# Kernel tuning notes

Measured on AMD Instinct MI355X. Metric: run time of the kernel, lower is better.

The kernel has to match this reference:

```python
import math
import jax, jax.numpy as jnp
import numpy as np

TOP_K = 2
N_EXP = 8
EVAL_CAPACITY_FACTOR = 2.0  # eval mode (module not training)
MIN_CAPACITY = 4


def _capacity(num_tokens):
    cap = math.floor(TOP_K * EVAL_CAPACITY_FACTOR * num_tokens / N_EXP)
    cap += cap % 2
    return max(cap, MIN_CAPACITY)


def setup_inputs() -> dict:
    key = jax.random.key(0)
    k1, k2 = jax.random.split(key)
    x = jax.random.normal(k1, (2, 2048, 1024), dtype=jnp.float32)
    w_g = jax.random.normal(k2, (8, 1024), dtype=jnp.float32) * 0.02
    return {"x": x, "w_g": w_g}


def reference(x, w_g):
    B, T, C = x.shape
    num_tokens = B * T
    cap = _capacity(num_tokens)  # static, derived from shapes

    # gating logits [B,T,E]
    logits = jnp.einsum('btc,ec->bte', x, w_g)

    # top-k + masked softmax (non-top-k logits -> -inf)
    top_logits, top_idx = jax.lax.top_k(logits, TOP_K)  # [B,T,K]
    masked = jnp.full_like(logits, -jnp.inf)
    masked = jnp.put_along_axis(masked, top_idx, top_logits, axis=-1, inplace=False)
    router_probs = jax.nn.softmax(masked, axis=-1)  # [B,T,E]

    # one-hot expert mask, ordered (k-major then token) for capacity ranking
    exp_mask = jax.nn.one_hot(top_idx, N_EXP, dtype=jnp.int32)       # [B,T,K,E]
    exp_mask = exp_mask.reshape(num_tokens, TOP_K, N_EXP)
    exp_mask = jnp.transpose(exp_mask, (1, 0, 2))                     # [K,tokens,E]

    # position of each assignment within its expert's queue
    exp_rank = jnp.cumsum(exp_mask.reshape(TOP_K * num_tokens, N_EXP), axis=0) - 1
    exp_rank = exp_rank.reshape(TOP_K, num_tokens, N_EXP)

    # drop assignments beyond capacity
    exp_mask = exp_mask * (exp_rank < cap).astype(jnp.int32)
    used_capacity = jnp.sum(exp_mask, axis=(0, 1))                    # [E]

    # per-assignment slot index [K,tokens]
    exp_rank = jnp.sum(exp_mask * exp_rank, axis=-1)

    rp = router_probs.reshape(num_tokens, N_EXP)[None, :, :]          # [1,tokens,E]
    exp_weights = exp_mask.astype(rp.dtype) * rp                      # [K,tokens,E]

    # one-hot over capacity slots -> combine weights [tokens,E,cap]
    exp_rank_sc = jax.nn.one_hot(exp_rank, cap, dtype=rp.dtype)       # [K,tokens,cap]
    cb_weight = jnp.sum(exp_weights[:, :, :, None] * exp_rank_sc[:, :, None, :], axis=0)
    sec_mask = cb_weight.astype(bool)
    return (used_capacity, cb_weight, sec_mask)
```

## Files before the change

kernel.cpp:

```cpp
#include <hip/hip_runtime.h>
#include <math.h>

#define TOKENS   4096
#define CDIM     1024
#define NEXP     8
#define CAP      2048
#define OUT_OFS  8
#define PER_OUT  (TOKENS * NEXP * CAP)
#define N4TOTAL  ((2 * PER_OUT + OUT_OFS) / 4)

#define GATE_BLOCKS   256
#define TOK_PER_WAVE  4
#define FILL_BLOCKS   ((N4TOTAL + 511) / 512)

__global__ __launch_bounds__(256) void fill_gate_kernel(const float* __restrict__ x,
                                                        const float* __restrict__ wg,
                                                        int*   __restrict__ top1,
                                                        int*   __restrict__ top2,
                                                        float* __restrict__ p1,
                                                        float* __restrict__ p2,
                                                        float4* __restrict__ out4) {
    if (blockIdx.x >= GATE_BLOCKS) {
        const int i = (blockIdx.x - GATE_BLOCKS) * 512 + threadIdx.x;
        const float4 z = make_float4(0.f, 0.f, 0.f, 0.f);
        if (i < N4TOTAL) out4[i] = z;
        const int i2 = i + 256;
        if (i2 < N4TOTAL) out4[i2] = z;
        return;
    }

    const int wave = threadIdx.x >> 6;
    const int lane = threadIdx.x & 63;

    for (int tt = 0; tt < TOK_PER_WAVE; ++tt) {
        const int tok = (blockIdx.x * 4 + wave) * TOK_PER_WAVE + tt;
        const float* xr = x + (size_t)tok * CDIM;

        float acc[NEXP];
#pragma unroll
        for (int e = 0; e < NEXP; ++e) acc[e] = 0.f;

#pragma unroll
        for (int i = 0; i < CDIM / 64; ++i) {
            const float xv = xr[lane + 64 * i];
#pragma unroll
            for (int e = 0; e < NEXP; ++e)
                acc[e] = fmaf(xv, wg[e * CDIM + lane + 64 * i], acc[e]);
        }
#pragma unroll
        for (int e = 0; e < NEXP; ++e) {
            float v = acc[e];
#pragma unroll
            for (int s = 32; s >= 1; s >>= 1) v += __shfl_xor(v, s, 64);
            acc[e] = v;
        }

        if (lane == 0) {
            int e1 = 0; float l1 = acc[0];
#pragma unroll
            for (int e = 1; e < NEXP; ++e)
                if (acc[e] > l1) { l1 = acc[e]; e1 = e; }
            int e2 = -1; float l2 = -INFINITY;
#pragma unroll
            for (int e = 0; e < NEXP; ++e)
                if (e != e1 && acc[e] > l2) { l2 = acc[e]; e2 = e; }
            const float ex = expf(l2 - l1);
            const float denom = 1.f + ex;
            top1[tok] = e1;
            top2[tok] = e2;
            p1[tok] = 1.f / denom;
            p2[tok] = ex / denom;
        }
    }
}

__global__ __launch_bounds__(256) void scan_scatter_kernel(const int* __restrict__ top1,
                                                           const int* __restrict__ top2,
                                                           const float* __restrict__ p1,
                                                           const float* __restrict__ p2,
                                                           float* __restrict__ out) {
    __shared__ int sr[2 * TOKENS];
    const int tid = threadIdx.x;

    if (tid < 64) {
        const int lane = tid;
        const int* __restrict__ src = (lane < 32) ? (top1 + lane * 128)
                                                  : (top2 + (lane - 32) * 128);
        int4 a[32];
#pragma unroll
        for (int i = 0; i < 32; ++i) a[i] = ((const int4*)src)[i];

        unsigned long long cnt = 0ull;
#pragma unroll
        for (int i = 0; i < 32; ++i) {
            cnt += 1ull << (a[i].x << 3);
            cnt += 1ull << (a[i].y << 3);
            cnt += 1ull << (a[i].z << 3);
            cnt += 1ull << (a[i].w << 3);
        }
        int c[NEXP];
#pragma unroll
        for (int e = 0; e < NEXP; ++e) c[e] = (int)((cnt >> (e * 8)) & 0xff);

        int off[NEXP], tot[NEXP];
#pragma unroll
        for (int e = 0; e < NEXP; ++e) {
            int v = c[e];
#pragma unroll
            for (int s = 1; s <= 32; s <<= 1) {
                const int u = __shfl_up(v, s, 64);
                if (lane >= s) v += u;
            }
            off[e] = v - c[e];
            tot[e] = __shfl(v, 63, 64);
        }

        int4* __restrict__ dst = (int4*)sr + lane * 32;
#pragma unroll
        for (int i = 0; i < 32; ++i) {
            int4 r;
            int e, rr;
            e = a[i].x; rr = 0;
#pragma unroll
            for (int ee = 0; ee < NEXP; ++ee) if (e == ee) { rr = off[ee]; off[ee] = rr + 1; }
            r.x = rr;
            e = a[i].y; rr = 0;
#pragma unroll
            for (int ee = 0; ee < NEXP; ++ee) if (e == ee) { rr = off[ee]; off[ee] = rr + 1; }
            r.y = rr;
            e = a[i].z; rr = 0;
#pragma unroll
            for (int ee = 0; ee < NEXP; ++ee) if (e == ee) { rr = off[ee]; off[ee] = rr + 1; }
            r.z = rr;
            e = a[i].w; rr = 0;
#pragma unroll
            for (int ee = 0; ee < NEXP; ++ee) if (e == ee) { rr = off[ee]; off[ee] = rr + 1; }
            r.w = rr;
            dst[i] = r;
        }

        if (lane < NEXP)
            out[lane] = (float)(tot[lane] < CAP ? tot[lane] : CAP);
    }
    __syncthreads();

    for (int a = tid; a < 2 * TOKENS; a += 256) {
        const int k = (a >= TOKENS);
        const int t = a & (TOKENS - 1);
        const int e = k ? top2[t] : top1[t];
        const int r = sr[a];
        const float p = k ? p2[t] : p1[t];
        if (r < CAP) {
            const size_t idx = ((size_t)t * NEXP + e) * CAP + r;
            out[OUT_OFS + idx] = p;
            out[OUT_OFS + (size_t)PER_OUT + idx] = (p != 0.f) ? 1.f : 0.f;
        }
    }
}

extern "C" void kernel_launch(void* const* d_in, const int* in_sizes, int n_in,
                              void* d_out, int out_size, void* d_ws, size_t ws_size,
                              hipStream_t stream) {
    const float* x  = (const float*)d_in[0];
    const float* wg = (const float*)d_in[1];
    float* out = (float*)d_out;

    int*   top1 = (int*)d_ws;
    int*   top2 = top1 + TOKENS;
    float* p1   = (float*)(top2 + TOKENS);
    float* p2   = p1 + TOKENS;

    fill_gate_kernel<<<GATE_BLOCKS + FILL_BLOCKS, 256, 0, stream>>>(
        x, wg, top1, top2, p1, p2, (float4*)out);

    scan_scatter_kernel<<<1, 256, 0, stream>>>(top1, top2, p1, p2, out);
}
```

Measured before the change: 132.2 us.

## Split output zero-fill into hipMemsetAsync and stage gate weights in LDS

Replaces the fused fill+gating kernel with a hipMemsetAsync that zeros the large output buffer, followed by a separate gating kernel that processes one token per wave. Each block first copies the 32KB gate weight matrix into shared memory before computing logits. The aim is a tuned driver fill path for the roughly 537MB zeroing and cheaper weight reads. The cost is that gating can no longer overlap with the fill, plus a per-block LDS staging step repeated across 1024 blocks.

```diff
diff --git a/kernel.cpp b/kernel.cpp
--- a/kernel.cpp
+++ b/kernel.cpp
@@ -7,70 +7,57 @@
 #define CAP      2048
 #define OUT_OFS  8
 #define PER_OUT  (TOKENS * NEXP * CAP)
-#define N4TOTAL  ((2 * PER_OUT + OUT_OFS) / 4)
 
-#define GATE_BLOCKS   256
-#define TOK_PER_WAVE  4
-#define FILL_BLOCKS   ((N4TOTAL + 511) / 512)
-
-__global__ __launch_bounds__(256) void fill_gate_kernel(const float* __restrict__ x,
-                                                        const float* __restrict__ wg,
-                                                        int*   __restrict__ top1,
-                                                        int*   __restrict__ top2,
-                                                        float* __restrict__ p1,
-                                                        float* __restrict__ p2,
-                                                        float4* __restrict__ out4) {
-    if (blockIdx.x >= GATE_BLOCKS) {
-        const int i = (blockIdx.x - GATE_BLOCKS) * 512 + threadIdx.x;
-        const float4 z = make_float4(0.f, 0.f, 0.f, 0.f);
-        if (i < N4TOTAL) out4[i] = z;
-        const int i2 = i + 256;
-        if (i2 < N4TOTAL) out4[i2] = z;
-        return;
-    }
+__global__ __launch_bounds__(256) void gating_kernel(const float* __restrict__ x,
+                                                     const float* __restrict__ wg,
+                                                     int*   __restrict__ top1,
+                                                     int*   __restrict__ top2,
+                                                     float* __restrict__ p1,
+                                                     float* __restrict__ p2) {
+    __shared__ float swg[NEXP * CDIM];
+    for (int i = threadIdx.x; i < NEXP * CDIM / 4; i += 256)
+        ((float4*)swg)[i] = ((const float4*)wg)[i];
+    __syncthreads();
 
     const int wave = threadIdx.x >> 6;
     const int lane = threadIdx.x & 63;
+    const int tok  = blockIdx.x * 4 + wave;
+    const float* xr = x + (size_t)tok * CDIM;
 
-    for (int tt = 0; tt < TOK_PER_WAVE; ++tt) {
-        const int tok = (blockIdx.x * 4 + wave) * TOK_PER_WAVE + tt;
-        const float* xr = x + (size_t)tok * CDIM;
-
-        float acc[NEXP];
+    float acc[NEXP];
 #pragma unroll
-        for (int e = 0; e < NEXP; ++e) acc[e] = 0.f;
+    for (int e = 0; e < NEXP; ++e) acc[e] = 0.f;
 
 #pragma unroll
-        for (int i = 0; i < CDIM / 64; ++i) {
-            const float xv = xr[lane + 64 * i];
+    for (int i = 0; i < CDIM / 64; ++i) {
+        const float xv = xr[lane + 64 * i];
 #pragma unroll
-            for (int e = 0; e < NEXP; ++e)
-                acc[e] = fmaf(xv, wg[e * CDIM + lane + 64 * i], acc[e]);
-        }
+        for (int e = 0; e < NEXP; ++e)
+            acc[e] = fmaf(xv, swg[e * CDIM + lane + 64 * i], acc[e]);
+    }
 #pragma unroll
-        for (int e = 0; e < NEXP; ++e) {
-            float v = acc[e];
+    for (int e = 0; e < NEXP; ++e) {
+        float v = acc[e];
 #pragma unroll
-            for (int s = 32; s >= 1; s >>= 1) v += __shfl_xor(v, s, 64);
-            acc[e] = v;
-        }
+        for (int s = 32; s >= 1; s >>= 1) v += __shfl_xor(v, s, 64);
+        acc[e] = v;
+    }
 
-        if (lane == 0) {
-            int e1 = 0; float l1 = acc[0];
+    if (lane == 0) {
+        int e1 = 0; float l1 = acc[0];
 #pragma unroll
-            for (int e = 1; e < NEXP; ++e)
-                if (acc[e] > l1) { l1 = acc[e]; e1 = e; }
-            int e2 = -1; float l2 = -INFINITY;
+        for (int e = 1; e < NEXP; ++e)
+            if (acc[e] > l1) { l1 = acc[e]; e1 = e; }
+        int e2 = -1; float l2 = -INFINITY;
 #pragma unroll
-            for (int e = 0; e < NEXP; ++e)
-                if (e != e1 && acc[e] > l2) { l2 = acc[e]; e2 = e; }
-            const float ex = expf(l2 - l1);
-            const float denom = 1.f + ex;
-            top1[tok] = e1;
-            top2[tok] = e2;
-            p1[tok] = 1.f / denom;
-            p2[tok] = ex / denom;
-        }
+        for (int e = 0; e < NEXP; ++e)
+            if (e != e1 && acc[e] > l2) { l2 = acc[e]; e2 = e; }
+        const float ex = expf(l2 - l1);
+        const float denom = 1.f + ex;
+        top1[tok] = e1;
+        top2[tok] = e2;
+        p1[tok] = 1.f / denom;
+        p2[tok] = ex / denom;
     }
 }
 
@@ -170,8 +157,9 @@
     float* p1   = (float*)(top2 + TOKENS);
     float* p2   = p1 + TOKENS;
 
-    fill_gate_kernel<<<GATE_BLOCKS + FILL_BLOCKS, 256, 0, stream>>>(
-        x, wg, top1, top2, p1, p2, (float4*)out);
+    hipMemsetAsync(out, 0, (size_t)(2 * PER_OUT + OUT_OFS) * sizeof(float), stream);
+
+    gating_kernel<<<TOKENS / 4, 256, 0, stream>>>(x, wg, top1, top2, p1, p2);
 
     scan_scatter_kernel<<<1, 256, 0, stream>>>(top1, top2, p1, p2, out);
 }
```

Result: faster. 126.1 us (-4.6%).
